# Performance work log

Hardware: AMD Instinct MI355X
Metric: run time of the kernel (lower is better)

## Reference

```python
import jax, jax.numpy as jnp
import numpy as np

NUM_GROUPS = 32
EPS = 1e-5


def group_norm(x, weight, bias):
    # x: (B, C, H, W, D); normalize per (group, spatial) per sample
    b, c, h, w, d = x.shape
    g = NUM_GROUPS
    xg = x.reshape(b, g, c // g, h, w, d)
    mean = xg.mean(axis=(2, 3, 4, 5), keepdims=True)
    var = xg.var(axis=(2, 3, 4, 5), keepdims=True)
    xg = (xg - mean) * jax.lax.rsqrt(var + EPS)
    xn = xg.reshape(b, c, h, w, d)
    return xn * weight[None, :, None, None, None] + bias[None, :, None, None, None]


def setup_inputs() -> dict:
    key = jax.random.key(0)
    ks = jax.random.split(key, 7)
    B, C, H, W, D = 4, 128, 16, 16, 16
    x = jax.random.normal(ks[0], (B, C, H, W, D), dtype=jnp.float32)
    gn_w = jnp.ones((C,), dtype=jnp.float32)
    gn_b = jnp.zeros((C,), dtype=jnp.float32)
    s = 1.0 / np.sqrt(C)
    qkv_w = jax.random.uniform(ks[1], (3 * C, C), minval=-s, maxval=s, dtype=jnp.float32)
    qkv_b = jax.random.uniform(ks[2], (3 * C,), minval=-s, maxval=s, dtype=jnp.float32)
    out_w = jax.random.uniform(ks[3], (C, C), minval=-s, maxval=s, dtype=jnp.float32)
    out_b = jax.random.uniform(ks[4], (C,), minval=-s, maxval=s, dtype=jnp.float32)
    return {"x": x, "gn_w": gn_w, "gn_b": gn_b, "qkv_w": qkv_w,
            "qkv_b": qkv_b, "out_w": out_w, "out_b": out_b}


def reference(x, gn_w, gn_b, qkv_w, qkv_b, out_w, out_b):
    b, c, h, w, d = x.shape
    n = h * w * d
    xn = group_norm(x, gn_w, gn_b)
    # 1x1x1 conv == pointwise linear over channels
    qkv = jnp.einsum('bchwd,oc->bohwd', xn, qkv_w) + qkv_b[None, :, None, None, None]
    q, k, v = jnp.split(qkv, 3, axis=1)
    q = q.transpose(0, 2, 3, 4, 1).reshape(b, n, c)   # (b, n, c)
    k = k.reshape(b, c, n)                             # (b, c, n)
    v = v.transpose(0, 2, 3, 4, 1).reshape(b, n, c)   # (b, n, c)
    scores = jnp.einsum('bnc,bcm->bnm', q, k) * (c ** -0.5)
    attn = jax.nn.softmax(scores, axis=-1)
    out = jnp.einsum('bnm,bmc->bnc', attn, v)          # (b, n, c)
    out = out.reshape(b, h, w, d, c).transpose(0, 4, 1, 2, 3)
    out = jnp.einsum('bchwd,oc->bohwd', out, out_w) + out_b[None, :, None, None, None]
    return out + x
```

## Files before the change

kernel.cpp:

```cpp
#include <hip/hip_runtime.h>

typedef unsigned short u16;
typedef __attribute__((ext_vector_type(8))) short bf16x8;
typedef __attribute__((ext_vector_type(4))) float f32x4;

__device__ __forceinline__ u16 f2bf(float f) {
    union { float f; unsigned u; } v; v.f = f;
    unsigned r = v.u + 0x7fffu + ((v.u >> 16) & 1u);
    return (u16)(r >> 16);
}

__device__ __forceinline__ void gload16(const u16* g, char* l) {
    __builtin_amdgcn_global_load_lds(
        (const __attribute__((address_space(1))) unsigned int*)g,
        (__attribute__((address_space(3))) unsigned int*)l, 16, 0, 0);
}

__global__ __launch_bounds__(256)
void k_stats(const float* __restrict__ x, float* __restrict__ mean, float* __restrict__ rstd)
{
    int bg = blockIdx.x, t = threadIdx.x;
    const float4* xp = (const float4*)(x + (size_t)bg * 16384);
    float s1 = 0.f, s2 = 0.f;
#pragma unroll
    for (int i = 0; i < 16; ++i) {
        float4 v = xp[i * 256 + t];
        s1 += v.x + v.y + v.z + v.w;
        s2 += v.x * v.x + v.y * v.y + v.z * v.z + v.w * v.w;
    }
#pragma unroll
    for (int off = 32; off >= 1; off >>= 1) {
        s1 += __shfl_xor(s1, off);
        s2 += __shfl_xor(s2, off);
    }
    __shared__ float a1[4], a2[4];
    if ((t & 63) == 0) { a1[t >> 6] = s1; a2[t >> 6] = s2; }
    __syncthreads();
    if (t == 0) {
        float t1 = a1[0] + a1[1] + a1[2] + a1[3];
        float t2 = a2[0] + a2[1] + a2[2] + a2[3];
        float mu = t1 * (1.f / 16384.f);
        float var = t2 * (1.f / 16384.f) - mu * mu;
        mean[bg] = mu;
        rstd[bg] = rsqrtf(var + 1e-5f);
    }
}

__global__ __launch_bounds__(384)
void k_qkv(const float* __restrict__ x, const float* __restrict__ gn_w, const float* __restrict__ gn_b,
           const float* __restrict__ qkv_w, const float* __restrict__ qkv_b,
           const float* __restrict__ mean, const float* __restrict__ rstd,
           u16* __restrict__ Qo, u16* __restrict__ Ko, u16* __restrict__ Vo)
{
    __shared__ float xn[128][64];
    int t = threadIdx.x;
    int b = blockIdx.x >> 6;
    int n0 = (blockIdx.x & 63) << 6;

    for (int e = t; e < 8192; e += 384) {
        int c = e >> 6, nn = e & 63;
        int bg = (b << 5) + (c >> 2);
        float sc = rstd[bg] * gn_w[c];
        float sh = gn_b[c] - mean[bg] * sc;
        xn[c][nn] = x[(size_t)(b * 128 + c) * 4096 + n0 + nn] * sc + sh;
    }
    __syncthreads();

    const int og = t >> 2;
    const int ng = t & 3;

    float acc[4][16];
#pragma unroll
    for (int i = 0; i < 4; ++i) {
        float bs = qkv_b[og * 4 + i];
#pragma unroll
        for (int j = 0; j < 16; ++j) acc[i][j] = bs;
    }

    const float4* wr0 = (const float4*)(qkv_w + (size_t)(og * 4 + 0) * 128);
    const float4* wr1 = (const float4*)(qkv_w + (size_t)(og * 4 + 1) * 128);
    const float4* wr2 = (const float4*)(qkv_w + (size_t)(og * 4 + 2) * 128);
    const float4* wr3 = (const float4*)(qkv_w + (size_t)(og * 4 + 3) * 128);

    for (int c4 = 0; c4 < 32; ++c4) {
        float4 w0 = wr0[c4], w1 = wr1[c4], w2 = wr2[c4], w3 = wr3[c4];
#pragma unroll
        for (int cc = 0; cc < 4; ++cc) {
            int c = c4 * 4 + cc;
            float v0 = (cc == 0) ? w0.x : (cc == 1) ? w0.y : (cc == 2) ? w0.z : w0.w;
            float v1 = (cc == 0) ? w1.x : (cc == 1) ? w1.y : (cc == 2) ? w1.z : w1.w;
            float v2 = (cc == 0) ? w2.x : (cc == 1) ? w2.y : (cc == 2) ? w2.z : w2.w;
            float v3 = (cc == 0) ? w3.x : (cc == 1) ? w3.y : (cc == 2) ? w3.z : w3.w;
#pragma unroll
            for (int j4 = 0; j4 < 4; ++j4) {
                float4 xv = *(const float4*)&xn[c][ng * 16 + j4 * 4];
#pragma unroll
                for (int jj = 0; jj < 4; ++jj) {
                    float xs = (jj == 0) ? xv.x : (jj == 1) ? xv.y : (jj == 2) ? xv.z : xv.w;
                    acc[0][j4 * 4 + jj] = fmaf(xs, v0, acc[0][j4 * 4 + jj]);
                    acc[1][j4 * 4 + jj] = fmaf(xs, v1, acc[1][j4 * 4 + jj]);
                    acc[2][j4 * 4 + jj] = fmaf(xs, v2, acc[2][j4 * 4 + jj]);
                    acc[3][j4 * 4 + jj] = fmaf(xs, v3, acc[3][j4 * 4 + jj]);
                }
            }
        }
    }

    const float qscale = 0.08838834764831845f * 1.4426950408889634f;
    if (og < 32) {
        size_t base = (size_t)(b * 4096 + n0 + ng * 16) * 128 + og * 4;
#pragma unroll
        for (int n = 0; n < 16; ++n) {
            uint2 pk;
            pk.x = ((unsigned)f2bf(acc[1][n] * qscale) << 16) | f2bf(acc[0][n] * qscale);
            pk.y = ((unsigned)f2bf(acc[3][n] * qscale) << 16) | f2bf(acc[2][n] * qscale);
            *(uint2*)&Qo[base + (size_t)n * 128] = pk;
        }
    } else if (og < 64) {
        size_t base = (size_t)(b * 4096 + n0 + ng * 16) * 128 + (og - 32) * 4;
#pragma unroll
        for (int n = 0; n < 16; ++n) {
            uint2 pk;
            pk.x = ((unsigned)f2bf(acc[1][n]) << 16) | f2bf(acc[0][n]);
            pk.y = ((unsigned)f2bf(acc[3][n]) << 16) | f2bf(acc[2][n]);
            *(uint2*)&Ko[base + (size_t)n * 128] = pk;
        }
    } else {
#pragma unroll
        for (int i = 0; i < 4; ++i) {
            size_t base = (size_t)(b * 128 + (og - 64) * 4 + i) * 4096 + n0 + ng * 16;
            uint4 pa, pb;
            pa.x = ((unsigned)f2bf(acc[i][1]) << 16) | f2bf(acc[i][0]);
            pa.y = ((unsigned)f2bf(acc[i][3]) << 16) | f2bf(acc[i][2]);
            pa.z = ((unsigned)f2bf(acc[i][5]) << 16) | f2bf(acc[i][4]);
            pa.w = ((unsigned)f2bf(acc[i][7]) << 16) | f2bf(acc[i][6]);
            pb.x = ((unsigned)f2bf(acc[i][9]) << 16) | f2bf(acc[i][8]);
            pb.y = ((unsigned)f2bf(acc[i][11]) << 16) | f2bf(acc[i][10]);
            pb.z = ((unsigned)f2bf(acc[i][13]) << 16) | f2bf(acc[i][12]);
            pb.w = ((unsigned)f2bf(acc[i][15]) << 16) | f2bf(acc[i][14]);
            *(uint4*)&Vo[base] = pa;
            *(uint4*)&Vo[base + 8] = pb;
        }
    }
}

__global__ __launch_bounds__(256, 2)
void k_attn(const u16* __restrict__ Qg, const u16* __restrict__ Kg, const u16* __restrict__ Vg,
            float* __restrict__ Opart, float* __restrict__ ml,
            int split, int kvlen, int iters)
{
    __shared__ __align__(16) u16 Kl[2][64 * 128];
    __shared__ __align__(16) u16 Vl[2][128 * 64];
    __shared__ __align__(16) u16 Pl[4 * 32 * 64];

    const int t = threadIdx.x;
    const int blk = blockIdx.x;
    const int half = blk % split;
    const int qt = (blk / split) & 31;
    const int b = blk / (split * 32);
    const int w = t >> 6;
    const int lane = t & 63;
    const int l15 = lane & 15;
    const int l4 = lane >> 4;
    const int q0 = qt << 7;
    const int swz = (l15 & 7) << 4;

    bf16x8 qf[2][4];
#pragma unroll
    for (int qh = 0; qh < 2; ++qh) {
        const u16* qb = Qg + (size_t)(b * 4096 + q0 + w * 32 + qh * 16 + l15) * 128 + l4 * 8;
#pragma unroll
        for (int kc = 0; kc < 4; ++kc) qf[qh][kc] = *(const bf16x8*)(qb + kc * 32);
    }
    f32x4 oac[2][8];
#pragma unroll
    for (int qh = 0; qh < 2; ++qh)
#pragma unroll
        for (int cf = 0; cf < 8; ++cf) oac[qh][cf] = (f32x4){0.f, 0.f, 0.f, 0.f};
    float m[2] = {-__builtin_inff(), -__builtin_inff()};
    float lsum[2] = {0.f, 0.f};

    const int kv0 = half * kvlen;
    char* plw = (char*)Pl + w * 4096;

    const int krow = lane >> 4;
    const int vrow = lane >> 3;
    const int kcolA = ((lane & 15) ^ krow) * 8;
    const int kcolB = ((lane & 15) ^ (krow + 4)) * 8;
    const int vcol  = ((lane & 7) ^ (vrow & 7)) * 8;
    const u16* KgB = Kg + (size_t)b * 4096 * 128;
    const u16* VgB = Vg + (size_t)b * 128 * 4096;

    auto STAGE = [&](int buf, int kvb) {
        char* kd = (char*)&Kl[buf][0] + w * 4096;
        char* vd = (char*)&Vl[buf][0] + w * 4096;
        const u16* kga = KgB + (size_t)(kvb + 16 * w) * 128;
        const u16* vga = VgB + kvb + (size_t)(32 * w) * 4096;
#pragma unroll
        for (int i = 0; i < 4; ++i) {
            gload16(kga + (size_t)(4 * i + krow) * 128 + ((i & 1) ? kcolB : kcolA),
                    kd + i * 1024);
            gload16(vga + (size_t)(8 * i + vrow) * 4096 + vcol,
                    vd + i * 1024);
        }
    };

    STAGE(0, kv0);
    __syncthreads();

    int cur = 0;
    for (int it = 0; it < iters; ++it) {
        if (it + 1 < iters) STAGE(cur ^ 1, kv0 + (it + 1) * 64);

        const char* kb = (const char*)&Kl[cur][0];
        f32x4 st[2][4];
        __builtin_amdgcn_s_setprio(1);
#pragma unroll
        for (int mt = 0; mt < 4; ++mt) {
            f32x4 s0 = (f32x4){0.f, 0.f, 0.f, 0.f};
            f32x4 s1 = (f32x4){0.f, 0.f, 0.f, 0.f};
#pragma unroll
            for (int kc = 0; kc < 4; ++kc) {
                bf16x8 kf = *(const bf16x8*)(kb + (mt * 16 + l15) * 256 +
                                             ((kc * 64 + l4 * 16) ^ swz));
                s0 = __builtin_amdgcn_mfma_f32_16x16x32_bf16(kf, qf[0][kc], s0, 0, 0, 0);
                s1 = __builtin_amdgcn_mfma_f32_16x16x32_bf16(kf, qf[1][kc], s1, 0, 0, 0);
            }
            st[0][mt] = s0;
            st[1][mt] = s1;
        }
        __builtin_amdgcn_s_setprio(0);

#pragma unroll
        for (int qh = 0; qh < 2; ++qh) {
            float pmax = -__builtin_inff();
#pragma unroll
            for (int mt = 0; mt < 4; ++mt)
                pmax = fmaxf(pmax, fmaxf(fmaxf(st[qh][mt][0], st[qh][mt][1]),
                                         fmaxf(st[qh][mt][2], st[qh][mt][3])));
            pmax = fmaxf(pmax, __shfl_xor(pmax, 16));
            pmax = fmaxf(pmax, __shfl_xor(pmax, 32));

            if (!__all(pmax - m[qh] <= 8.f)) {
                float nm = fmaxf(m[qh], pmax);
                float fr = __builtin_amdgcn_exp2f(m[qh] - nm);
                m[qh] = nm;
                lsum[qh] *= fr;
#pragma unroll
                for (int cf = 0; cf < 8; ++cf)
#pragma unroll
                    for (int r = 0; r < 4; ++r) oac[qh][cf][r] *= fr;
            }

            float rsum = 0.f;
            uint2 pw[4];
#pragma unroll
            for (int mt = 0; mt < 4; ++mt) {
                float p0 = __builtin_amdgcn_exp2f(st[qh][mt][0] - m[qh]);
                float p1 = __builtin_amdgcn_exp2f(st[qh][mt][1] - m[qh]);
                float p2 = __builtin_amdgcn_exp2f(st[qh][mt][2] - m[qh]);
                float p3 = __builtin_amdgcn_exp2f(st[qh][mt][3] - m[qh]);
                rsum += (p0 + p1) + (p2 + p3);
                pw[mt].x = ((unsigned)f2bf(p1) << 16) | f2bf(p0);
                pw[mt].y = ((unsigned)f2bf(p3) << 16) | f2bf(p2);
            }
            rsum += __shfl_xor(rsum, 16);
            rsum += __shfl_xor(rsum, 32);
            lsum[qh] += rsum;

#pragma unroll
            for (int mt = 0; mt < 4; ++mt)
                *(uint2*)(plw + (qh * 16 + l15) * 128 + ((mt * 32 + l4 * 8) ^ swz)) = pw[mt];
        }
        asm volatile("s_waitcnt lgkmcnt(0)" ::: "memory");
        __builtin_amdgcn_sched_barrier(0);

        const char* vb = (const char*)&Vl[cur][0];
        __builtin_amdgcn_s_setprio(1);
#pragma unroll
        for (int kc2 = 0; kc2 < 2; ++kc2) {
            bf16x8 pf0 = *(const bf16x8*)(plw + (0 * 16 + l15) * 128 + ((kc2 * 64 + l4 * 16) ^ swz));
            bf16x8 pf1 = *(const bf16x8*)(plw + (1 * 16 + l15) * 128 + ((kc2 * 64 + l4 * 16) ^ swz));
#pragma unroll
            for (int cf = 0; cf < 8; ++cf) {
                bf16x8 vf = *(const bf16x8*)(vb + (cf * 16 + l15) * 128 +
                                             ((kc2 * 64 + l4 * 16) ^ swz));
                oac[0][cf] = __builtin_amdgcn_mfma_f32_16x16x32_bf16(vf, pf0, oac[0][cf], 0, 0, 0);
                oac[1][cf] = __builtin_amdgcn_mfma_f32_16x16x32_bf16(vf, pf1, oac[1][cf], 0, 0, 0);
            }
        }
        __builtin_amdgcn_s_setprio(0);
        __syncthreads();
        cur ^= 1;
    }

#pragma unroll
    for (int qh = 0; qh < 2; ++qh) {
        size_t qrow = ((size_t)half * 4 + b) * 4096 + q0 + w * 32 + qh * 16 + l15;
        float* orow = Opart + qrow * 128;
#pragma unroll
        for (int cf = 0; cf < 8; ++cf) {
            float4 v;
            v.x = oac[qh][cf][0]; v.y = oac[qh][cf][1];
            v.z = oac[qh][cf][2]; v.w = oac[qh][cf][3];
            *(float4*)&orow[cf * 16 + l4 * 4] = v;
        }
        if (l4 == 0) {
            size_t mb = (size_t)half * 16384 + b * 4096 + q0 + w * 32 + qh * 16 + l15;
            ml[mb * 2 + 0] = m[qh];
            ml[mb * 2 + 1] = lsum[qh];
        }
    }
}

__global__ __launch_bounds__(256)
void k_proj(const float* __restrict__ Opart, const float* __restrict__ ml,
            const float* __restrict__ x, const float* __restrict__ out_w,
            const float* __restrict__ out_b, float* __restrict__ out, int split)
{
    __shared__ float Ol[128][64];
    int t = threadIdx.x;
    int b = blockIdx.x >> 6;
    int n0 = (blockIdx.x & 63) << 6;

    for (int e = t; e < 2048; e += 256) {
        int nn = e >> 5, c4 = e & 31;
        size_t rg = (size_t)b * 4096 + n0 + nn;
        float msv[4], lsv[4];
#pragma unroll
        for (int s = 0; s < 4; ++s) {
            if (s < split) {
                msv[s] = ml[((size_t)s * 16384 + rg) * 2 + 0];
                lsv[s] = ml[((size_t)s * 16384 + rg) * 2 + 1];
            } else { msv[s] = -__builtin_inff(); lsv[s] = 0.f; }
        }
        float mm = fmaxf(fmaxf(msv[0], msv[1]), fmaxf(msv[2], msv[3]));
        float es[4]; float L = 0.f;
#pragma unroll
        for (int s = 0; s < 4; ++s) {
            es[s] = (s < split) ? __builtin_amdgcn_exp2f(msv[s] - mm) : 0.f;
            L += lsv[s] * es[s];
        }
        float inv = 1.f / L;
        float ox = 0.f, oy = 0.f, oz = 0.f, ow = 0.f;
#pragma unroll
        for (int s = 0; s < 4; ++s) {
            if (s < split) {
                float4 o4 = *(const float4*)&Opart[((size_t)s * 16384 + rg) * 128 + c4 * 4];
                ox = fmaf(o4.x, es[s], ox); oy = fmaf(o4.y, es[s], oy);
                oz = fmaf(o4.z, es[s], oz); ow = fmaf(o4.w, es[s], ow);
            }
        }
        Ol[c4 * 4 + 0][nn] = ox * inv;
        Ol[c4 * 4 + 1][nn] = oy * inv;
        Ol[c4 * 4 + 2][nn] = oz * inv;
        Ol[c4 * 4 + 3][nn] = ow * inv;
    }
    __syncthreads();

    const int ocg = t & 31;
    const int ng = t >> 5;

    float acc[4][8];
#pragma unroll
    for (int i = 0; i < 4; ++i) {
        float bs = out_b[ocg * 4 + i];
#pragma unroll
        for (int j = 0; j < 8; ++j) acc[i][j] = bs;
    }

    const float4* wr0 = (const float4*)(out_w + (size_t)(ocg * 4 + 0) * 128);
    const float4* wr1 = (const float4*)(out_w + (size_t)(ocg * 4 + 1) * 128);
    const float4* wr2 = (const float4*)(out_w + (size_t)(ocg * 4 + 2) * 128);
    const float4* wr3 = (const float4*)(out_w + (size_t)(ocg * 4 + 3) * 128);

    for (int c4 = 0; c4 < 32; ++c4) {
        float4 w0 = wr0[c4], w1 = wr1[c4], w2 = wr2[c4], w3 = wr3[c4];
#pragma unroll
        for (int cc = 0; cc < 4; ++cc) {
            int c = c4 * 4 + cc;
            float v0 = (cc == 0) ? w0.x : (cc == 1) ? w0.y : (cc == 2) ? w0.z : w0.w;
            float v1 = (cc == 0) ? w1.x : (cc == 1) ? w1.y : (cc == 2) ? w1.z : w1.w;
            float v2 = (cc == 0) ? w2.x : (cc == 1) ? w2.y : (cc == 2) ? w2.z : w2.w;
            float v3 = (cc == 0) ? w3.x : (cc == 1) ? w3.y : (cc == 2) ? w3.z : w3.w;
#pragma unroll
            for (int j4 = 0; j4 < 2; ++j4) {
                float4 xv = *(const float4*)&Ol[c][ng * 8 + j4 * 4];
#pragma unroll
                for (int jj = 0; jj < 4; ++jj) {
                    float xs = (jj == 0) ? xv.x : (jj == 1) ? xv.y : (jj == 2) ? xv.z : xv.w;
                    acc[0][j4 * 4 + jj] = fmaf(xs, v0, acc[0][j4 * 4 + jj]);
                    acc[1][j4 * 4 + jj] = fmaf(xs, v1, acc[1][j4 * 4 + jj]);
                    acc[2][j4 * 4 + jj] = fmaf(xs, v2, acc[2][j4 * 4 + jj]);
                    acc[3][j4 * 4 + jj] = fmaf(xs, v3, acc[3][j4 * 4 + jj]);
                }
            }
        }
    }

#pragma unroll
    for (int i = 0; i < 4; ++i) {
        size_t ob = (size_t)(b * 128 + ocg * 4 + i) * 4096 + n0 + ng * 8;
#pragma unroll
        for (int j4 = 0; j4 < 2; ++j4) {
            float4 xr = *(const float4*)&x[ob + j4 * 4];
            float4 ov;
            ov.x = acc[i][j4 * 4 + 0] + xr.x;
            ov.y = acc[i][j4 * 4 + 1] + xr.y;
            ov.z = acc[i][j4 * 4 + 2] + xr.z;
            ov.w = acc[i][j4 * 4 + 3] + xr.w;
            *(float4*)&out[ob + j4 * 4] = ov;
        }
    }
}

extern "C" void kernel_launch(void* const* d_in, const int* in_sizes, int n_in,
                              void* d_out, int out_size, void* d_ws, size_t ws_size,
                              hipStream_t stream)
{
    const float* x     = (const float*)d_in[0];
    const float* gn_w  = (const float*)d_in[1];
    const float* gn_b  = (const float*)d_in[2];
    const float* qkv_w = (const float*)d_in[3];
    const float* qkv_b = (const float*)d_in[4];
    const float* out_w = (const float*)d_in[5];
    const float* out_b = (const float*)d_in[6];
    float* out = (float*)d_out;

    char* ws = (char*)d_ws;
    float* mean  = (float*)ws;
    float* rstd  = (float*)(ws + 512);
    u16*   Q     = (u16*)(ws + 4096);
    u16*   K     = (u16*)(ws + 4198400);
    u16*   V     = (u16*)(ws + 8392704);
    float* mlb   = (float*)(ws + 12587008);
    float* Opart = (float*)(ws + 13111296);

    int split = (ws_size >= (size_t)46700000) ? 4 : 2;
    int kvlen = 4096 / split;
    int iters = kvlen / 64;

    k_stats<<<128, 256, 0, stream>>>(x, mean, rstd);
    k_qkv<<<256, 384, 0, stream>>>(x, gn_w, gn_b, qkv_w, qkv_b, mean, rstd, Q, K, V);
    k_attn<<<128 * split, 256, 0, stream>>>(Q, K, V, Opart, mlb, split, kvlen, iters);
    k_proj<<<256, 256, 0, stream>>>(Opart, mlb, x, out_w, out_b, out, split);
}
```

Before: 126.9 us.

## Use bf16 MFMA for QKV projection, halve proj tiles, drop attention waitcnt

The QKV projection moves from scalar fp32 FMAs to bf16 MFMA 16x16x32. Normalized activations are staged in swizzled bf16 shared memory, and weights are converted to bf16 on the fly. The output projection kernel now uses 32-row tiles over twice as many blocks, with a row-major padded shared buffer. An explicit lgkmcnt wait and sched barrier are removed from the attention inner loop. Together these aim to cut projection compute time and raise occupancy, at the cost of bf16 rounding of the weights and activations. Removing the wait could race on the P tile in LDS.

```diff
diff --git a/kernel.cpp b/kernel.cpp
--- a/kernel.cpp
+++ b/kernel.cpp
@@ -46,100 +46,112 @@
     }
 }
 
-__global__ __launch_bounds__(384)
+__global__ __launch_bounds__(256)
 void k_qkv(const float* __restrict__ x, const float* __restrict__ gn_w, const float* __restrict__ gn_b,
            const float* __restrict__ qkv_w, const float* __restrict__ qkv_b,
            const float* __restrict__ mean, const float* __restrict__ rstd,
            u16* __restrict__ Qo, u16* __restrict__ Ko, u16* __restrict__ Vo)
 {
-    __shared__ float xn[128][64];
-    int t = threadIdx.x;
-    int b = blockIdx.x >> 6;
-    int n0 = (blockIdx.x & 63) << 6;
-
-    for (int e = t; e < 8192; e += 384) {
+    __shared__ float xnf[128][65];
+    __shared__ __align__(16) u16 xb[64 * 128];
+    const int t = threadIdx.x;
+    const int b = blockIdx.x >> 6;
+    const int n0 = (blockIdx.x & 63) << 6;
+
+    for (int i = 0; i < 32; ++i) {
+        int e = i * 256 + t;
         int c = e >> 6, nn = e & 63;
         int bg = (b << 5) + (c >> 2);
         float sc = rstd[bg] * gn_w[c];
         float sh = gn_b[c] - mean[bg] * sc;
-        xn[c][nn] = x[(size_t)(b * 128 + c) * 4096 + n0 + nn] * sc + sh;
+        xnf[c][nn] = x[(size_t)(b * 128 + c) * 4096 + n0 + nn] * sc + sh;
     }
     __syncthreads();
 
-    const int og = t >> 2;
-    const int ng = t & 3;
-
-    float acc[4][16];
-#pragma unroll
-    for (int i = 0; i < 4; ++i) {
-        float bs = qkv_b[og * 4 + i];
-#pragma unroll
-        for (int j = 0; j < 16; ++j) acc[i][j] = bs;
-    }
-
-    const float4* wr0 = (const float4*)(qkv_w + (size_t)(og * 4 + 0) * 128);
-    const float4* wr1 = (const float4*)(qkv_w + (size_t)(og * 4 + 1) * 128);
-    const float4* wr2 = (const float4*)(qkv_w + (size_t)(og * 4 + 2) * 128);
-    const float4* wr3 = (const float4*)(qkv_w + (size_t)(og * 4 + 3) * 128);
-
-    for (int c4 = 0; c4 < 32; ++c4) {
-        float4 w0 = wr0[c4], w1 = wr1[c4], w2 = wr2[c4], w3 = wr3[c4];
-#pragma unroll
-        for (int cc = 0; cc < 4; ++cc) {
-            int c = c4 * 4 + cc;
-            float v0 = (cc == 0) ? w0.x : (cc == 1) ? w0.y : (cc == 2) ? w0.z : w0.w;
-            float v1 = (cc == 0) ? w1.x : (cc == 1) ? w1.y : (cc == 2) ? w1.z : w1.w;
-            float v2 = (cc == 0) ? w2.x : (cc == 1) ? w2.y : (cc == 2) ? w2.z : w2.w;
-            float v3 = (cc == 0) ? w3.x : (cc == 1) ? w3.y : (cc == 2) ? w3.z : w3.w;
-#pragma unroll
-            for (int j4 = 0; j4 < 4; ++j4) {
-                float4 xv = *(const float4*)&xn[c][ng * 16 + j4 * 4];
-#pragma unroll
-                for (int jj = 0; jj < 4; ++jj) {
-                    float xs = (jj == 0) ? xv.x : (jj == 1) ? xv.y : (jj == 2) ? xv.z : xv.w;
-                    acc[0][j4 * 4 + jj] = fmaf(xs, v0, acc[0][j4 * 4 + jj]);
-                    acc[1][j4 * 4 + jj] = fmaf(xs, v1, acc[1][j4 * 4 + jj]);
-                    acc[2][j4 * 4 + jj] = fmaf(xs, v2, acc[2][j4 * 4 + jj]);
-                    acc[3][j4 * 4 + jj] = fmaf(xs, v3, acc[3][j4 * 4 + jj]);
-                }
-            }
+    {
+        int nn = t >> 2;
+        int k0 = (t & 3) * 16;
+        char* row = (char*)xb + nn * 256;
+        int sw = (nn & 7) << 4;
+#pragma unroll
+        for (int i = 0; i < 16; ++i) {
+            int k = k0 + i;
+            float lo = xnf[2 * k][nn], hi = xnf[2 * k + 1][nn];
+            *(unsigned*)(row + ((4 * k) ^ sw)) = ((unsigned)f2bf(hi) << 16) | f2bf(lo);
+        }
+    }
+    __syncthreads();
+
+    const int w = t >> 6, lane = t & 63, l15 = lane & 15, l4 = lane >> 4;
+    const int swz = (l15 & 7) << 4;
+
+    f32x4 acc[6][4];
+#pragma unroll
+    for (int T = 0; T < 6; ++T) {
+        int ot = w + T * 4;
+        float4 bs = *(const float4*)&qkv_b[ot * 16 + l4 * 4];
+#pragma unroll
+        for (int nt = 0; nt < 4; ++nt)
+            acc[T][nt] = (f32x4){bs.x, bs.y, bs.z, bs.w};
+    }
+
+#pragma unroll 1
+    for (int kc = 0; kc < 4; ++kc) {
+        bf16x8 bf[4];
+#pragma unroll
+        for (int nt = 0; nt < 4; ++nt)
+            bf[nt] = *(const bf16x8*)((char*)xb + (nt * 16 + l15) * 256 +
+                                      ((kc * 64 + l4 * 16) ^ swz));
+#pragma unroll
+        for (int T = 0; T < 6; ++T) {
+            int ot = w + T * 4;
+            const float* wp = qkv_w + (size_t)(ot * 16 + l15) * 128 + kc * 32 + l4 * 8;
+            float4 wa = *(const float4*)wp;
+            float4 wb = *(const float4*)(wp + 4);
+            bf16x8 wf;
+            wf[0] = (short)f2bf(wa.x); wf[1] = (short)f2bf(wa.y);
+            wf[2] = (short)f2bf(wa.z); wf[3] = (short)f2bf(wa.w);
+            wf[4] = (short)f2bf(wb.x); wf[5] = (short)f2bf(wb.y);
+            wf[6] = (short)f2bf(wb.z); wf[7] = (short)f2bf(wb.w);
+#pragma unroll
+            for (int nt = 0; nt < 4; ++nt)
+                acc[T][nt] = __builtin_amdgcn_mfma_f32_16x16x32_bf16(wf, bf[nt], acc[T][nt], 0, 0, 0);
         }
     }
 
     const float qscale = 0.08838834764831845f * 1.4426950408889634f;
-    if (og < 32) {
-        size_t base = (size_t)(b * 4096 + n0 + ng * 16) * 128 + og * 4;
-#pragma unroll
-        for (int n = 0; n < 16; ++n) {
-            uint2 pk;
-            pk.x = ((unsigned)f2bf(acc[1][n] * qscale) << 16) | f2bf(acc[0][n] * qscale);
-            pk.y = ((unsigned)f2bf(acc[3][n] * qscale) << 16) | f2bf(acc[2][n] * qscale);
-            *(uint2*)&Qo[base + (size_t)n * 128] = pk;
-        }
-    } else if (og < 64) {
-        size_t base = (size_t)(b * 4096 + n0 + ng * 16) * 128 + (og - 32) * 4;
-#pragma unroll
-        for (int n = 0; n < 16; ++n) {
-            uint2 pk;
-            pk.x = ((unsigned)f2bf(acc[1][n]) << 16) | f2bf(acc[0][n]);
-            pk.y = ((unsigned)f2bf(acc[3][n]) << 16) | f2bf(acc[2][n]);
-            *(uint2*)&Ko[base + (size_t)n * 128] = pk;
-        }
-    } else {
-#pragma unroll
-        for (int i = 0; i < 4; ++i) {
-            size_t base = (size_t)(b * 128 + (og - 64) * 4 + i) * 4096 + n0 + ng * 16;
-            uint4 pa, pb;
-            pa.x = ((unsigned)f2bf(acc[i][1]) << 16) | f2bf(acc[i][0]);
-            pa.y = ((unsigned)f2bf(acc[i][3]) << 16) | f2bf(acc[i][2]);
-            pa.z = ((unsigned)f2bf(acc[i][5]) << 16) | f2bf(acc[i][4]);
-            pa.w = ((unsigned)f2bf(acc[i][7]) << 16) | f2bf(acc[i][6]);
-            pb.x = ((unsigned)f2bf(acc[i][9]) << 16) | f2bf(acc[i][8]);
-            pb.y = ((unsigned)f2bf(acc[i][11]) << 16) | f2bf(acc[i][10]);
-            pb.z = ((unsigned)f2bf(acc[i][13]) << 16) | f2bf(acc[i][12]);
-            pb.w = ((unsigned)f2bf(acc[i][15]) << 16) | f2bf(acc[i][14]);
-            *(uint4*)&Vo[base] = pa;
-            *(uint4*)&Vo[base + 8] = pb;
+#pragma unroll
+    for (int T = 0; T < 6; ++T) {
+        int ot = w + T * 4;
+        if (ot < 8) {
+            int o = ot * 16 + l4 * 4;
+#pragma unroll
+            for (int nt = 0; nt < 4; ++nt) {
+                int n = n0 + nt * 16 + l15;
+                uint2 pk;
+                pk.x = ((unsigned)f2bf(acc[T][nt][1] * qscale) << 16) | f2bf(acc[T][nt][0] * qscale);
+                pk.y = ((unsigned)f2bf(acc[T][nt][3] * qscale) << 16) | f2bf(acc[T][nt][2] * qscale);
+                *(uint2*)&Qo[(size_t)(b * 4096 + n) * 128 + o] = pk;
+            }
+        } else if (ot < 16) {
+            int o = (ot - 8) * 16 + l4 * 4;
+#pragma unroll
+            for (int nt = 0; nt < 4; ++nt) {
+                int n = n0 + nt * 16 + l15;
+                uint2 pk;
+                pk.x = ((unsigned)f2bf(acc[T][nt][1]) << 16) | f2bf(acc[T][nt][0]);
+                pk.y = ((unsigned)f2bf(acc[T][nt][3]) << 16) | f2bf(acc[T][nt][2]);
+                *(uint2*)&Ko[(size_t)(b * 4096 + n) * 128 + o] = pk;
+            }
+        } else {
+            int o = (ot - 16) * 16 + l4 * 4;
+#pragma unroll
+            for (int nt = 0; nt < 4; ++nt) {
+                int n = n0 + nt * 16 + l15;
+#pragma unroll
+                for (int r = 0; r < 4; ++r)
+                    Vo[(size_t)(b * 128 + o + r) * 4096 + n] = f2bf(acc[T][nt][r]);
+            }
         }
     }
 }
@@ -272,8 +284,6 @@
             for (int mt = 0; mt < 4; ++mt)
                 *(uint2*)(plw + (qh * 16 + l15) * 128 + ((mt * 32 + l4 * 8) ^ swz)) = pw[mt];
         }
-        asm volatile("s_waitcnt lgkmcnt(0)" ::: "memory");
-        __builtin_amdgcn_sched_barrier(0);
 
         const char* vb = (const char*)&Vl[cur][0];
         __builtin_amdgcn_s_setprio(1);
@@ -318,55 +328,58 @@
             const float* __restrict__ x, const float* __restrict__ out_w,
             const float* __restrict__ out_b, float* __restrict__ out, int split)
 {
-    __shared__ float Ol[128][64];
-    int t = threadIdx.x;
-    int b = blockIdx.x >> 6;
-    int n0 = (blockIdx.x & 63) << 6;
-
-    for (int e = t; e < 2048; e += 256) {
-        int nn = e >> 5, c4 = e & 31;
-        size_t rg = (size_t)b * 4096 + n0 + nn;
-        float msv[4], lsv[4];
-#pragma unroll
-        for (int s = 0; s < 4; ++s) {
-            if (s < split) {
-                msv[s] = ml[((size_t)s * 16384 + rg) * 2 + 0];
-                lsv[s] = ml[((size_t)s * 16384 + rg) * 2 + 1];
-            } else { msv[s] = -__builtin_inff(); lsv[s] = 0.f; }
-        }
-        float mm = fmaxf(fmaxf(msv[0], msv[1]), fmaxf(msv[2], msv[3]));
-        float es[4]; float L = 0.f;
-#pragma unroll
-        for (int s = 0; s < 4; ++s) {
-            es[s] = (s < split) ? __builtin_amdgcn_exp2f(msv[s] - mm) : 0.f;
-            L += lsv[s] * es[s];
-        }
-        float inv = 1.f / L;
-        float ox = 0.f, oy = 0.f, oz = 0.f, ow = 0.f;
-#pragma unroll
-        for (int s = 0; s < 4; ++s) {
-            if (s < split) {
-                float4 o4 = *(const float4*)&Opart[((size_t)s * 16384 + rg) * 128 + c4 * 4];
-                ox = fmaf(o4.x, es[s], ox); oy = fmaf(o4.y, es[s], oy);
-                oz = fmaf(o4.z, es[s], oz); ow = fmaf(o4.w, es[s], ow);
-            }
-        }
-        Ol[c4 * 4 + 0][nn] = ox * inv;
-        Ol[c4 * 4 + 1][nn] = oy * inv;
-        Ol[c4 * 4 + 2][nn] = oz * inv;
-        Ol[c4 * 4 + 3][nn] = ow * inv;
+    __shared__ float Ol[32][132];
+    const int t = threadIdx.x;
+    const int b = blockIdx.x >> 7;
+    const int n0 = (blockIdx.x & 127) << 5;
+
+    {
+        int c4 = t & 31;
+        int nb = t >> 5;
+#pragma unroll
+        for (int i = 0; i < 4; ++i) {
+            int nn = i * 8 + nb;
+            size_t rg = (size_t)b * 4096 + n0 + nn;
+            float msv[4], lsv[4];
+#pragma unroll
+            for (int s = 0; s < 4; ++s) {
+                if (s < split) {
+                    msv[s] = ml[((size_t)s * 16384 + rg) * 2 + 0];
+                    lsv[s] = ml[((size_t)s * 16384 + rg) * 2 + 1];
+                } else { msv[s] = -__builtin_inff(); lsv[s] = 0.f; }
+            }
+            float mm = fmaxf(fmaxf(msv[0], msv[1]), fmaxf(msv[2], msv[3]));
+            float es[4]; float L = 0.f;
+#pragma unroll
+            for (int s = 0; s < 4; ++s) {
+                es[s] = (s < split) ? __builtin_amdgcn_exp2f(msv[s] - mm) : 0.f;
+                L += lsv[s] * es[s];
+            }
+            float inv = 1.f / L;
+            float ox = 0.f, oy = 0.f, oz = 0.f, ow = 0.f;
+#pragma unroll
+            for (int s = 0; s < 4; ++s) {
+                if (s < split) {
+                    float4 o4 = *(const float4*)&Opart[((size_t)s * 16384 + rg) * 128 + c4 * 4];
+                    ox = fmaf(o4.x, es[s], ox); oy = fmaf(o4.y, es[s], oy);
+                    oz = fmaf(o4.z, es[s], oz); ow = fmaf(o4.w, es[s], ow);
+                }
+            }
+            float4 res; res.x = ox * inv; res.y = oy * inv; res.z = oz * inv; res.w = ow * inv;
+            *(float4*)&Ol[nn][c4 * 4] = res;
+        }
     }
     __syncthreads();
 
     const int ocg = t & 31;
     const int ng = t >> 5;
 
-    float acc[4][8];
+    float acc[4][4];
 #pragma unroll
     for (int i = 0; i < 4; ++i) {
         float bs = out_b[ocg * 4 + i];
 #pragma unroll
-        for (int j = 0; j < 8; ++j) acc[i][j] = bs;
+        for (int j = 0; j < 4; ++j) acc[i][j] = bs;
     }
 
     const float4* wr0 = (const float4*)(out_w + (size_t)(ocg * 4 + 0) * 128);
@@ -376,41 +389,41 @@
 
     for (int c4 = 0; c4 < 32; ++c4) {
         float4 w0 = wr0[c4], w1 = wr1[c4], w2 = wr2[c4], w3 = wr3[c4];
+        float4 xv0 = *(const float4*)&Ol[ng * 4 + 0][c4 * 4];
+        float4 xv1 = *(const float4*)&Ol[ng * 4 + 1][c4 * 4];
+        float4 xv2 = *(const float4*)&Ol[ng * 4 + 2][c4 * 4];
+        float4 xv3 = *(const float4*)&Ol[ng * 4 + 3][c4 * 4];
 #pragma unroll
         for (int cc = 0; cc < 4; ++cc) {
-            int c = c4 * 4 + cc;
             float v0 = (cc == 0) ? w0.x : (cc == 1) ? w0.y : (cc == 2) ? w0.z : w0.w;
             float v1 = (cc == 0) ? w1.x : (cc == 1) ? w1.y : (cc == 2) ? w1.z : w1.w;
             float v2 = (cc == 0) ? w2.x : (cc == 1) ? w2.y : (cc == 2) ? w2.z : w2.w;
             float v3 = (cc == 0) ? w3.x : (cc == 1) ? w3.y : (cc == 2) ? w3.z : w3.w;
-#pragma unroll
-            for (int j4 = 0; j4 < 2; ++j4) {
-                float4 xv = *(const float4*)&Ol[c][ng * 8 + j4 * 4];
-#pragma unroll
-                for (int jj = 0; jj < 4; ++jj) {
-                    float xs = (jj == 0) ? xv.x : (jj == 1) ? xv.y : (jj == 2) ? xv.z : xv.w;
-                    acc[0][j4 * 4 + jj] = fmaf(xs, v0, acc[0][j4 * 4 + jj]);
-                    acc[1][j4 * 4 + jj] = fmaf(xs, v1, acc[1][j4 * 4 + jj]);
-                    acc[2][j4 * 4 + jj] = fmaf(xs, v2, acc[2][j4 * 4 + jj]);
-                    acc[3][j4 * 4 + jj] = fmaf(xs, v3, acc[3][j4 * 4 + jj]);
-                }
-            }
+            float x0 = (cc == 0) ? xv0.x : (cc == 1) ? xv0.y : (cc == 2) ? xv0.z : xv0.w;
+            float x1 = (cc == 0) ? xv1.x : (cc == 1) ? xv1.y : (cc == 2) ? xv1.z : xv1.w;
+            float x2 = (cc == 0) ? xv2.x : (cc == 1) ? xv2.y : (cc == 2) ? xv2.z : xv2.w;
+            float x3 = (cc == 0) ? xv3.x : (cc == 1) ? xv3.y : (cc == 2) ? xv3.z : xv3.w;
+            acc[0][0] = fmaf(x0, v0, acc[0][0]); acc[0][1] = fmaf(x1, v0, acc[0][1]);
+            acc[0][2] = fmaf(x2, v0, acc[0][2]); acc[0][3] = fmaf(x3, v0, acc[0][3]);
+            acc[1][0] = fmaf(x0, v1, acc[1][0]); acc[1][1] = fmaf(x1, v1, acc[1][1]);
+            acc[1][2] = fmaf(x2, v1, acc[1][2]); acc[1][3] = fmaf(x3, v1, acc[1][3]);
+            acc[2][0] = fmaf(x0, v2, acc[2][0]); acc[2][1] = fmaf(x1, v2, acc[2][1]);
+            acc[2][2] = fmaf(x2, v2, acc[2][2]); acc[2][3] = fmaf(x3, v2, acc[2][3]);
+            acc[3][0] = fmaf(x0, v3, acc[3][0]); acc[3][1] = fmaf(x1, v3, acc[3][1]);
+            acc[3][2] = fmaf(x2, v3, acc[3][2]); acc[3][3] = fmaf(x3, v3, acc[3][3]);
         }
     }
 
 #pragma unroll
     for (int i = 0; i < 4; ++i) {
-        size_t ob = (size_t)(b * 128 + ocg * 4 + i) * 4096 + n0 + ng * 8;
-#pragma unroll
-        for (int j4 = 0; j4 < 2; ++j4) {
-            float4 xr = *(const float4*)&x[ob + j4 * 4];
-            float4 ov;
-            ov.x = acc[i][j4 * 4 + 0] + xr.x;
-            ov.y = acc[i][j4 * 4 + 1] + xr.y;
-            ov.z = acc[i][j4 * 4 + 2] + xr.z;
-            ov.w = acc[i][j4 * 4 + 3] + xr.w;
-            *(float4*)&out[ob + j4 * 4] = ov;
-        }
+        size_t ob = (size_t)(b * 128 + ocg * 4 + i) * 4096 + n0 + ng * 4;
+        float4 xr = *(const float4*)&x[ob];
+        float4 ov;
+        ov.x = acc[i][0] + xr.x;
+        ov.y = acc[i][1] + xr.y;
+        ov.z = acc[i][2] + xr.z;
+        ov.w = acc[i][3] + xr.w;
+        *(float4*)&out[ob] = ov;
     }
 }
 
@@ -441,7 +454,7 @@
     int iters = kvlen / 64;
 
     k_stats<<<128, 256, 0, stream>>>(x, mean, rstd);
-    k_qkv<<<256, 384, 0, stream>>>(x, gn_w, gn_b, qkv_w, qkv_b, mean, rstd, Q, K, V);
+    k_qkv<<<256, 256, 0, stream>>>(x, gn_w, gn_b, qkv_w, qkv_b, mean, rstd, Q, K, V);
     k_attn<<<128 * split, 256, 0, stream>>>(Q, K, V, Opart, mlb, split, kvlen, iters);
-    k_proj<<<256, 256, 0, stream>>>(Opart, mlb, x, out_w, out_b, out, split);
-}
+    k_proj<<<512, 256, 0, stream>>>(Opart, mlb, x, out_w, out_b, out, split);
+}
```

Measured after the change: 132.8 us. 4.6% more time.
